# Performance work log

Hardware: AMD Instinct MI355X
Metric: run time of the kernel (lower is better)

## Reference

```python
import jax, jax.numpy as jnp
import numpy as np

N_NODES = 20000
N_EDGES = 160000
N_GRAPHS = 100
IN_CH = 64
EDGE_DIM = 8
NEG_SLOPE = 0.2


def _gatv2(x, edge_index, edge_attr, Wl, Wr, We, att, b, heads, ch, n_nodes):
    # GATv2Conv: e_ij = att . leaky_relu(Wl x_j + Wr x_i [+ We e_ij]), softmax over dst i,
    # out_i = sum_j alpha_ij * (Wl x_j), concat heads, + bias.
    src, dst = edge_index[0], edge_index[1]
    xl = (x @ Wl).reshape(-1, heads, ch)  # [N,H,C] source-side transform
    xr = (x @ Wr).reshape(-1, heads, ch)  # [N,H,C] target-side transform
    m = xl[src] + xr[dst]                 # [E,H,C]
    if edge_attr is not None:
        m = m + (edge_attr @ We).reshape(-1, heads, ch)
    m = jax.nn.leaky_relu(m, NEG_SLOPE)
    logit = jnp.einsum('ehc,hc->eh', m, att)                     # [E,H]
    mx = jax.ops.segment_max(logit, dst, num_segments=n_nodes)   # [N,H]
    ex = jnp.exp(logit - mx[dst])
    den = jax.ops.segment_sum(ex, dst, num_segments=n_nodes)     # [N,H]
    alpha = ex / (den[dst] + 1e-16)                              # [E,H]
    out = jax.ops.segment_sum(alpha[:, :, None] * xl[src], dst, num_segments=n_nodes)
    return out.reshape(-1, heads * ch) + b


def setup_inputs() -> dict:
    key = jax.random.key(0)
    ks = jax.random.split(key, 24)
    def rn(k, shape, fan_in):
        return jax.random.normal(k, shape, dtype=jnp.float32) / np.sqrt(fan_in)
    inp = {}
    inp['x'] = jax.random.normal(ks[0], (N_NODES, IN_CH), dtype=jnp.float32)
    inp['edge_attr'] = jax.random.uniform(ks[1], (N_EDGES, EDGE_DIM), dtype=jnp.float32)
    inp['Wl1'] = rn(ks[2], (IN_CH, 1024), IN_CH)
    inp['Wr1'] = rn(ks[3], (IN_CH, 1024), IN_CH)
    inp['We1'] = rn(ks[4], (EDGE_DIM, 1024), EDGE_DIM)
    inp['att1'] = rn(ks[5], (4, 256), 256)
    inp['b1'] = jnp.zeros((1024,), jnp.float32)
    inp['Wl2'] = rn(ks[6], (1024, 256), 1024)
    inp['Wr2'] = rn(ks[7], (1024, 256), 1024)
    inp['We2'] = rn(ks[8], (EDGE_DIM, 256), EDGE_DIM)
    inp['att2'] = rn(ks[9], (4, 64), 64)
    inp['b2'] = jnp.zeros((256,), jnp.float32)
    inp['Wlp'] = rn(ks[10], (256, 384), 256)
    inp['Wrp'] = rn(ks[11], (256, 384), 256)
    inp['attp'] = rn(ks[12], (6, 64), 64)
    inp['bp'] = jnp.zeros((384,), jnp.float32)
    inp['Wfc1'] = rn(ks[13], (384, 64), 384)
    inp['bfc1'] = jnp.zeros((64,), jnp.float32)
    inp['Wfc2'] = rn(ks[14], (64, 1), 64)
    inp['bfc2'] = jnp.zeros((1,), jnp.float32)
    inp['edge_index'] = jax.random.randint(ks[15], (2, N_EDGES), 0, N_NODES, dtype=jnp.int32)
    inp['edge_index_master'] = jax.random.randint(ks[16], (2, N_EDGES), 0, N_NODES, dtype=jnp.int32)
    inp['n_nodes'] = jnp.full((N_GRAPHS,), N_NODES // N_GRAPHS, dtype=jnp.int32)
    return inp


def reference(x, edge_attr, Wl1, Wr1, We1, att1, b1, Wl2, Wr2, We2, att2, b2,
              Wlp, Wrp, attp, bp, Wfc1, bfc1, Wfc2, bfc2,
              edge_index, edge_index_master, n_nodes):
    h = _gatv2(x, edge_index, edge_attr, Wl1, Wr1, We1, att1, b1, 4, 256, N_NODES)
    h = jax.nn.relu(h)
    h = _gatv2(h, edge_index, edge_attr, Wl2, Wr2, We2, att2, b2, 4, 64, N_NODES)
    h = jax.nn.relu(h)
    h = _gatv2(h, edge_index_master, None, Wlp, Wrp, None, attp, bp, 6, 64, N_NODES)
    last_idx = jnp.cumsum(n_nodes) - 1          # master node = last node of each graph
    master = h[last_idx]                        # [G,384] (dropout p=0 -> identity)
    z = jax.nn.relu(master @ Wfc1 + bfc1)
    return z @ Wfc2 + bfc2                      # [G,1]
```

## Files before the change

### kernel.cpp

```cpp
#include <hip/hip_runtime.h>
#include <hip/hip_bf16.h>

#define DIV_UP(a,b) (((a)+(b)-1)/(b))

typedef __attribute__((ext_vector_type(8))) short short8;
typedef __attribute__((ext_vector_type(4))) float floatx4;

static __device__ __forceinline__ unsigned short f2bf(float v) {
    unsigned u = __builtin_bit_cast(unsigned, v);
    u += 0x7fffu + ((u >> 16) & 1u);
    return (unsigned short)(u >> 16);
}
static __device__ __forceinline__ float bflo(unsigned v) {
    return __builtin_bit_cast(float, v << 16);
}
static __device__ __forceinline__ float bfhi(unsigned v) {
    return __builtin_bit_cast(float, v & 0xffff0000u);
}
static __device__ __forceinline__ float fexp2(float x) { return __builtin_amdgcn_exp2f(x); }
static __device__ __forceinline__ float f4get(const float4 v, int k) {
    return k == 0 ? v.x : k == 1 ? v.y : k == 2 ? v.z : v.w;
}

template <int CPL> struct RawT;
template <> struct RawT<8> { using T = uint4; };
template <> struct RawT<4> { using T = uint2; };
template <> struct RawT<2> { using T = unsigned; };

template <int CPL>
static __device__ __forceinline__ void unpackx(const typename RawT<CPL>::T& v, float* d) {
    if constexpr (CPL == 8) {
        d[0] = bflo(v.x); d[1] = bfhi(v.x);
        d[2] = bflo(v.y); d[3] = bfhi(v.y);
        d[4] = bflo(v.z); d[5] = bfhi(v.z);
        d[6] = bflo(v.w); d[7] = bfhi(v.w);
    } else if constexpr (CPL == 4) {
        d[0] = bflo(v.x); d[1] = bfhi(v.x);
        d[2] = bflo(v.y); d[3] = bfhi(v.y);
    } else {
        d[0] = bflo(v); d[1] = bfhi(v);
    }
}

template <int CPL>
static __device__ __forceinline__ void store_bf16v(unsigned short* p, const float* s) {
    unsigned short tmp[CPL];
#pragma unroll
    for (int c = 0; c < CPL; ++c) tmp[c] = f2bf(s[c]);
    if constexpr (CPL == 8) *(uint4*)p = *(uint4*)tmp;
    else if constexpr (CPL == 4) *(ushort4*)p = *(ushort4*)tmp;
    else if constexpr (CPL == 2) *(ushort2*)p = *(ushort2*)tmp;
    else p[0] = tmp[0];
}

template <int CTRL>
static __device__ __forceinline__ float dpp_mv(float x) {
    int r = __builtin_amdgcn_update_dpp(0, __builtin_bit_cast(int, x), CTRL, 0xF, 0xF, false);
    return __builtin_bit_cast(float, r);
}
template <int G>
static __device__ __forceinline__ float group_reduce(float x) {
    x += dpp_mv<0xB1>(x);
    x += dpp_mv<0x4E>(x);
    x += dpp_mv<0x124>(x);
    x += dpp_mv<0x128>(x);
    if constexpr (G >= 32) x += __shfl_xor(x, 16, 64);
    if constexpr (G >= 64) x += __shfl_xor(x, 32, 64);
    return x;
}

static __device__ __forceinline__ void tr_pair(const float* Wa, const float* Wb, int K, int Nn,
                                               unsigned short* Wt, int i) {
    int tot = K * Nn;
    const float* W = (i < tot) ? Wa : Wb;
    unsigned short* dst = Wt + ((i < tot) ? 0 : (size_t)Nn * K);
    int ii = (i < tot) ? i : i - tot;
    int k = ii % K, n = ii / K;
    dst[(size_t)n * K + k] = f2bf(W[(size_t)k * Nn + n]);
}

__global__ void prep_all(const float* __restrict__ x,
                         const float* __restrict__ Wl1, const float* __restrict__ Wr1,
                         const float* __restrict__ Wl2, const float* __restrict__ Wr2,
                         const float* __restrict__ Wlp, const float* __restrict__ Wrp,
                         unsigned short* __restrict__ xbf,
                         unsigned short* __restrict__ wt1, unsigned short* __restrict__ wt2,
                         unsigned short* __restrict__ wt3, int N) {
    const int S1 = 2 * 64 * 1024, S2 = 2 * 1024 * 256, S3 = 2 * 256 * 384;
    int id = blockIdx.x * blockDim.x + threadIdx.x;
    if (id < S1) tr_pair(Wl1, Wr1, 64, 1024, wt1, id);
    else if (id < S1 + S2) tr_pair(Wl2, Wr2, 1024, 256, wt2, id - S1);
    else if (id < S1 + S2 + S3) tr_pair(Wlp, Wrp, 256, 384, wt3, id - S1 - S2);
    else {
        int i = id - S1 - S2 - S3;
        if (i < N * 64) xbf[i] = f2bf(x[i]);
    }
}

#define GLOAD_LDS16(gp, lp) \
    __builtin_amdgcn_global_load_lds((const __attribute__((address_space(1))) void*)(gp), \
                                     (__attribute__((address_space(3))) void*)(lp), 16, 0, 0)

__global__ __launch_bounds__(256) void gemm_mfma(
    const unsigned short* __restrict__ A, const unsigned short* __restrict__ Bt,
    unsigned short* __restrict__ C, int M, int Ntot, int K) {
    __shared__ unsigned short As[128 * 32];
    __shared__ unsigned short Bs[128 * 32];
    const int tid = threadIdx.x;
    const int m0 = blockIdx.y * 128, n0 = blockIdx.x * 128;
    const int wave = tid >> 6, lane = tid & 63;
    const int wm = (wave >> 1) * 64, wn = (wave & 1) * 64;
    const int r15 = lane & 15, quad = lane >> 4;
    const int srow = lane >> 2, scol = (lane & 3) * 8;
    const int arow0 = m0 + 32 * wave + srow;
    const int brow0 = n0 + 32 * wave + srow;
    const unsigned short* ap0 = A + (size_t)arow0 * K + scol;
    const unsigned short* ap1 = ap0 + (size_t)16 * K;
    const unsigned short* bp0 = Bt + (size_t)brow0 * K + scol;
    const unsigned short* bp1 = bp0 + (size_t)16 * K;
    unsigned short* alds0 = As + (32 * wave) * 32;
    unsigned short* alds1 = alds0 + 16 * 32;
    unsigned short* blds0 = Bs + (32 * wave) * 32;
    unsigned short* blds1 = blds0 + 16 * 32;
    const bool av0 = arow0 < M, av1 = (arow0 + 16) < M;
    floatx4 acc[4][4];
#pragma unroll
    for (int i = 0; i < 4; ++i)
#pragma unroll
        for (int j = 0; j < 4; ++j) acc[i][j] = (floatx4)0.f;

    for (int k0 = 0; k0 < K; k0 += 32) {
        if (av0) GLOAD_LDS16(ap0, alds0);
        if (av1) GLOAD_LDS16(ap1, alds1);
        GLOAD_LDS16(bp0, blds0);
        GLOAD_LDS16(bp1, blds1);
        ap0 += 32; ap1 += 32; bp0 += 32; bp1 += 32;
        __syncthreads();
        short8 af[4], bfr[4];
#pragma unroll
        for (int i = 0; i < 4; ++i)
            af[i] = *(const short8*)(&As[(wm + i * 16 + r15) * 32 + quad * 8]);
#pragma unroll
        for (int j = 0; j < 4; ++j)
            bfr[j] = *(const short8*)(&Bs[(wn + j * 16 + r15) * 32 + quad * 8]);
#pragma unroll
        for (int i = 0; i < 4; ++i)
#pragma unroll
            for (int j = 0; j < 4; ++j)
                acc[i][j] = __builtin_amdgcn_mfma_f32_16x16x32_bf16(af[i], bfr[j], acc[i][j], 0, 0, 0);
        __syncthreads();
    }
#pragma unroll
    for (int i = 0; i < 4; ++i)
#pragma unroll
        for (int j = 0; j < 4; ++j)
#pragma unroll
            for (int r = 0; r < 4; ++r) {
                int m = m0 + wm + i * 16 + quad * 4 + r;
                int n = n0 + wn + j * 16 + r15;
                if (m < M) C[(size_t)m * Ntot + n] = f2bf(acc[i][j][r]);
            }
}

__global__ void count2_kernel(const int* __restrict__ dst0, const int* __restrict__ dst1,
                              int E, int N, int* __restrict__ cnt) {
    int e = blockIdx.x * blockDim.x + threadIdx.x;
    if (e < E) atomicAdd(&cnt[dst0[e]], 1);
    else if (e < 2 * E) atomicAdd(&cnt[N + dst1[e - E]], 1);
}

__global__ __launch_bounds__(1024) void scan_kernel(const int* __restrict__ cnt_all, int N,
                                                    int* __restrict__ off_all, int* __restrict__ cur_all) {
    const int* cnt = cnt_all + blockIdx.x * N;
    int* off = off_all + blockIdx.x * (N + 1);
    int* cur = cur_all + blockIdx.x * N;
    __shared__ int part[1024];
    int t = threadIdx.x;
    int per = (N + 1023) >> 10;
    int base = t * per;
    int s = 0;
    for (int i = 0; i < per; ++i) { int idx = base + i; if (idx < N) s += cnt[idx]; }
    part[t] = s;
    __syncthreads();
    for (int d2 = 1; d2 < 1024; d2 <<= 1) {
        int v = (t >= d2) ? part[t - d2] : 0;
        __syncthreads();
        part[t] += v;
        __syncthreads();
    }
    int pre = (t == 0) ? 0 : part[t - 1];
    for (int i = 0; i < per; ++i) {
        int idx = base + i;
        if (idx < N) { off[idx] = pre; cur[idx] = pre; pre += cnt[idx]; }
    }
    if (t == 1023) off[N] = part[1023];
}

__global__ void fill2_kernel(const int* __restrict__ src0, const int* __restrict__ dst0,
                             const int* __restrict__ src1, const int* __restrict__ dst1,
                             int E, int N, int* __restrict__ cur, int2* __restrict__ edges,
                             int* __restrict__ srcs) {
    int e = blockIdx.x * blockDim.x + threadIdx.x;
    if (e < E) {
        int p = atomicAdd(&cur[dst0[e]], 1);
        edges[p] = make_int2(src0[e], e);
        srcs[p] = src0[e];
    } else if (e < 2 * E) {
        int i = e - E;
        int p = atomicAdd(&cur[N + dst1[i]], 1);
        srcs[E + p] = src1[i];
    }
}

__global__ void ea_gather_kernel(const float* __restrict__ ea, const int2* __restrict__ edges,
                                 float* __restrict__ ead, int E) {
    int j = blockIdx.x * blockDim.x + threadIdx.x;
    if (j >= E) return;
    int ey = edges[j].y;
    const float4* s = (const float4*)(ea + (size_t)ey * 8);
    float4* o = (float4*)(ead + (size_t)j * 8);
    o[0] = s[0];
    o[1] = s[1];
}

template <int CPL, int NE>
struct EStage {
    int src[NE];
    typename RawT<CPL>::T xv[NE];
};

template <int D, int CPL, int NE>
static __device__ __forceinline__ void stage_x(
    const unsigned short* __restrict__ xlr, const int* __restrict__ srcs,
    int j, int c0, EStage<CPL, NE>& s) {
#pragma unroll
    for (int n = 0; n < NE; ++n) s.src[n] = srcs[j + n];
#pragma unroll
    for (int n = 0; n < NE; ++n)
        s.xv[n] = *(const typename RawT<CPL>::T*)(xlr + (size_t)s.src[n] * (2 * D) + c0);
}

template <int D, int CPL, int QP, int G, int NE>
static __device__ __forceinline__ void hase_compute(
    const EStage<CPL, NE>& s, const float* __restrict__ ead, int j,
    const float* wb, const float (&att_r)[CPL], const float (&xr_r)[CPL],
    float& m, float& l, float (&acc)[CPL]) {
    float4 evr[NE][2];
#pragma unroll
    for (int n = 0; n < NE; ++n) {
        const float4* q = (const float4*)(ead + (size_t)(j + n) * 8);
        evr[n][0] = q[0];
        evr[n][1] = q[1];
    }
    float z[NE][CPL];
#pragma unroll
    for (int n = 0; n < NE; ++n) {
        float xv[CPL];
        unpackx<CPL>(s.xv[n], xv);
#pragma unroll
        for (int c = 0; c < CPL; ++c) z[n][c] = xv[c] + xr_r[c];
    }
#pragma unroll
    for (int k = 0; k < 8; ++k) {
#pragma unroll
        for (int q = 0; q < CPL / 4; ++q) {
            float4 w4 = *(const float4*)(wb + k * D + q * QP);
#pragma unroll
            for (int n = 0; n < NE; ++n) {
                float ek = f4get(evr[n][k >> 2], k & 3);
                z[n][q * 4 + 0] = fmaf(ek, w4.x, z[n][q * 4 + 0]);
                z[n][q * 4 + 1] = fmaf(ek, w4.y, z[n][q * 4 + 1]);
                z[n][q * 4 + 2] = fmaf(ek, w4.z, z[n][q * 4 + 2]);
                z[n][q * 4 + 3] = fmaf(ek, w4.w, z[n][q * 4 + 3]);
            }
        }
    }
    float lg[NE];
#pragma unroll
    for (int n = 0; n < NE; ++n) {
        float t = 0.f;
#pragma unroll
        for (int c = 0; c < CPL; ++c) {
            float a = z[n][c] > 0.f ? z[n][c] : 0.2f * z[n][c];
            t = fmaf(att_r[c], a, t);
        }
        lg[n] = group_reduce<G>(t);
    }
    float mn = m;
#pragma unroll
    for (int n = 0; n < NE; ++n) mn = fmaxf(mn, lg[n]);
    float sc = fexp2(m - mn);
    float p[NE], ps = 0.f;
#pragma unroll
    for (int n = 0; n < NE; ++n) { p[n] = fexp2(lg[n] - mn); ps += p[n]; }
    m = mn;
    l = fmaf(l, sc, ps);
#pragma unroll
    for (int c = 0; c < CPL; ++c) acc[c] *= sc;
#pragma unroll
    for (int n = 0; n < NE; ++n) {
        float xv[CPL];
        unpackx<CPL>(s.xv[n], xv);
#pragma unroll
        for (int c = 0; c < CPL; ++c) acc[c] = fmaf(p[n], xv[c], acc[c]);
    }
}

template <int D, int C, int CB, int WPN, bool RELU>
__global__ __launch_bounds__(256) void attn_hase(
    const unsigned short* __restrict__ xlr, const float* __restrict__ ead,
    const float* __restrict__ We, const float* __restrict__ att,
    const int* __restrict__ srcs, const int* __restrict__ off,
    const float* __restrict__ bias, unsigned short* __restrict__ outp, int N) {
    constexpr int CPL = CB / 64;
    constexpr int HW = CB / C;
    constexpr int G = 64 / HW;
    constexpr int NPB = 4 / WPN;
    constexpr int QP = CB * 4 / CPL;
    __shared__ float wsh[8 * D];
    for (int f4 = threadIdx.x; f4 < 2 * D; f4 += 256) {
        int k = f4 / (D / 4);
        int c = (f4 - k * (D / 4)) * 4;
        int b = c / CB, cc = c - b * CB;
        int ln = cc / CPL, q = (cc % CPL) / 4;
        int dst = k * (D / 4) + (b * CB + q * QP + ln * 4) / 4;
        ((float4*)wsh)[dst] = ((const float4*)We)[f4];
    }
    __syncthreads();

    const int wid = threadIdx.x >> 6, lane = threadIdx.x & 63;
    const int wv = wid % WPN, wn = wid / WPN;
    const int c0 = wv * CB + lane * CPL;
    const float* wb = wsh + wv * CB + lane * 4;

    const float L2E = 1.4426950408889634f;
    float att_r[CPL];
#pragma unroll
    for (int c = 0; c < CPL; ++c) att_r[c] = att[c0 + c] * L2E;

    for (int node = blockIdx.x * NPB + wn; node < N; node += gridDim.x * NPB) {
        typename RawT<CPL>::T xrw =
            *(const typename RawT<CPL>::T*)(xlr + (size_t)node * (2 * D) + D + c0);
        float xr_r[CPL];
        unpackx<CPL>(xrw, xr_r);
        float m = -1e30f, l = 0.f, acc[CPL];
#pragma unroll
        for (int c = 0; c < CPL; ++c) acc[c] = 0.f;

        const int jb = __builtin_amdgcn_readfirstlane(off[node]);
        const int je = __builtin_amdgcn_readfirstlane(off[node + 1]);
        int j = jb;
        int g = (je - jb) >> 2;
        if (g > 0) {
            EStage<CPL, 4> A, B;
            stage_x<D, CPL, 4>(xlr, srcs, j, c0, A);
            while (g >= 2) {
                stage_x<D, CPL, 4>(xlr, srcs, j + 4, c0, B);
                hase_compute<D, CPL, QP, G, 4>(A, ead, j, wb, att_r, xr_r, m, l, acc);
                j += 4; --g;
                if (g >= 2) {
                    stage_x<D, CPL, 4>(xlr, srcs, j + 4, c0, A);
                    hase_compute<D, CPL, QP, G, 4>(B, ead, j, wb, att_r, xr_r, m, l, acc);
                    j += 4; --g;
                } else if (g == 1) {
                    hase_compute<D, CPL, QP, G, 4>(B, ead, j, wb, att_r, xr_r, m, l, acc);
                    j += 4; --g;
                }
            }
            if (g == 1) {
                hase_compute<D, CPL, QP, G, 4>(A, ead, j, wb, att_r, xr_r, m, l, acc);
                j += 4;
            }
        }
        for (; j < je; ++j) {
            EStage<CPL, 1> S;
            stage_x<D, CPL, 1>(xlr, srcs, j, c0, S);
            hase_compute<D, CPL, QP, G, 1>(S, ead, j, wb, att_r, xr_r, m, l, acc);
        }

        float inv = 1.f / (l + 1e-16f);
        float r[CPL];
#pragma unroll
        for (int c = 0; c < CPL; ++c) {
            r[c] = fmaf(acc[c], inv, bias[c0 + c]);
            if constexpr (RELU) r[c] = fmaxf(r[c], 0.f);
        }
        store_bf16v<CPL>(outp + (size_t)node * D + c0, r);
    }
}

template <int D, int CPL, int G, int NE>
static __device__ __forceinline__ void noe_compute(
    const EStage<CPL, NE>& s,
    const float (&att_r)[CPL], const float (&xr_r)[CPL],
    float& m, float& l, float (&acc)[CPL]) {
    float xv[NE][CPL], lg[NE];
#pragma unroll
    for (int n = 0; n < NE; ++n) unpackx<CPL>(s.xv[n], xv[n]);
#pragma unroll
    for (int n = 0; n < NE; ++n) {
        float t = 0.f;
#pragma unroll
        for (int c = 0; c < CPL; ++c) {
            float z = xv[n][c] + xr_r[c];
            z = z > 0.f ? z : 0.2f * z;
            t = fmaf(att_r[c], z, t);
        }
        lg[n] = group_reduce<G>(t);
    }
    float mn = m;
#pragma unroll
    for (int n = 0; n < NE; ++n) mn = fmaxf(mn, lg[n]);
    float sc = fexp2(m - mn);
    float p[NE], ps = 0.f;
#pragma unroll
    for (int n = 0; n < NE; ++n) { p[n] = fexp2(lg[n] - mn); ps += p[n]; }
    m = mn;
    l = fmaf(l, sc, ps);
#pragma unroll
    for (int c = 0; c < CPL; ++c) {
        float t = p[0] * xv[0][c];
#pragma unroll
        for (int n = 1; n < NE; ++n) t = fmaf(p[n], xv[n][c], t);
        acc[c] = fmaf(acc[c], sc, t);
    }
}

template <int D, int C, int CB, bool RELU>
static __device__ __forceinline__ void attn_wave3(
    const unsigned short* __restrict__ xlr, const float* __restrict__ att,
    const int* __restrict__ srcs, int jb, int je,
    const float* __restrict__ bias, float* __restrict__ outp,
    int node, int cb, int lane) {
    constexpr int CPL = CB / 64;
    constexpr int HW = CB / C;
    constexpr int G = 64 / HW;
    const int c0 = cb + lane * CPL;
    const float L2E = 1.4426950408889634f;

    typename RawT<CPL>::T xrw =
        *(const typename RawT<CPL>::T*)(xlr + (size_t)node * (2 * D) + D + c0);
    float xr_r[CPL], att_r[CPL];
    unpackx<CPL>(xrw, xr_r);
#pragma unroll
    for (int c = 0; c < CPL; ++c) att_r[c] = att[c0 + c] * L2E;

    float m = -1e30f, l = 0.f, acc[CPL];
#pragma unroll
    for (int c = 0; c < CPL; ++c) acc[c] = 0.f;

    int j = jb;
    int g = (je - jb) >> 2;
    if (g > 0) {
        EStage<CPL, 4> A, B;
        stage_x<D, CPL, 4>(xlr, srcs, j, c0, A);
        while (g >= 2) {
            stage_x<D, CPL, 4>(xlr, srcs, j + 4, c0, B);
            noe_compute<D, CPL, G, 4>(A, att_r, xr_r, m, l, acc);
            j += 4; --g;
            if (g >= 2) {
                stage_x<D, CPL, 4>(xlr, srcs, j + 4, c0, A);
                noe_compute<D, CPL, G, 4>(B, att_r, xr_r, m, l, acc);
                j += 4; --g;
            } else if (g == 1) {
                noe_compute<D, CPL, G, 4>(B, att_r, xr_r, m, l, acc);
                j += 4; --g;
            }
        }
        if (g == 1) {
            noe_compute<D, CPL, G, 4>(A, att_r, xr_r, m, l, acc);
            j += 4;
        }
    }
    for (; j < je; ++j) {
        EStage<CPL, 1> S;
        stage_x<D, CPL, 1>(xlr, srcs, j, c0, S);
        noe_compute<D, CPL, G, 1>(S, att_r, xr_r, m, l, acc);
    }

    float inv = 1.f / (l + 1e-16f);
    float* out = outp + (size_t)node * D + c0;
    float tmp[CPL];
#pragma unroll
    for (int c = 0; c < CPL; ++c) {
        float r = fmaf(acc[c], inv, bias[c0 + c]);
        if constexpr (RELU) r = fmaxf(r, 0.f);
        tmp[c] = r;
    }
    if constexpr (CPL == 4) *(float4*)out = *(float4*)tmp;
    else if constexpr (CPL == 2) *(float2*)out = *(float2*)tmp;
    else out[0] = tmp[0];
}

template <int D, int C, int CB0, int CB1, bool RELU>
__global__ __launch_bounds__(256) void attn_noe(
    const unsigned short* __restrict__ xlr, const float* __restrict__ att,
    const int* __restrict__ srcs, const int* __restrict__ off,
    const float* __restrict__ bias, float* __restrict__ outp, int N) {
    const int wid = threadIdx.x >> 6, lane = threadIdx.x & 63;
    const int gw = blockIdx.x * 4 + wid;
    const int node = gw >> 1, wv = gw & 1;
    if (node >= N) return;
    const int jb = __builtin_amdgcn_readfirstlane(off[node]);
    const int je = __builtin_amdgcn_readfirstlane(off[node + 1]);
    if (wv == 0)
        attn_wave3<D, C, CB0, RELU>(xlr, att, srcs, jb, je, bias, outp, node, 0, lane);
    else
        attn_wave3<D, C, CB1, RELU>(xlr, att, srcs, jb, je, bias, outp, node, CB0, lane);
}

__global__ void mlp_kernel(const float* __restrict__ h3, const int* __restrict__ nn,
                           const float* __restrict__ Wfc1, const float* __restrict__ bfc1,
                           const float* __restrict__ Wfc2, const float* __restrict__ bfc2,
                           float* __restrict__ out, int G) {
    int g = blockIdx.x, t = threadIdx.x;
    int s = 0;
    for (int k = 0; k <= g; ++k) s += nn[k];
    const float* row = h3 + (size_t)(s - 1) * 384;
    float z = bfc1[t];
    for (int k = 0; k < 384; ++k) z = fmaf(row[k], Wfc1[k * 64 + t], z);
    z = fmaxf(z, 0.f);
    float v = z * Wfc2[t];
#pragma unroll
    for (int o = 32; o; o >>= 1) v += __shfl_xor(v, o, 64);
    if (t == 0) out[g] = v + bfc2[0];
}

extern "C" void kernel_launch(void* const* d_in, const int* in_sizes, int n_in,
                              void* d_out, int out_size, void* d_ws, size_t ws_size,
                              hipStream_t stream) {
    const float* x    = (const float*)d_in[0];
    const float* ea   = (const float*)d_in[1];
    const float* Wl1  = (const float*)d_in[2];
    const float* Wr1  = (const float*)d_in[3];
    const float* We1  = (const float*)d_in[4];
    const float* att1 = (const float*)d_in[5];
    const float* b1   = (const float*)d_in[6];
    const float* Wl2  = (const float*)d_in[7];
    const float* Wr2  = (const float*)d_in[8];
    const float* We2  = (const float*)d_in[9];
    const float* att2 = (const float*)d_in[10];
    const float* b2   = (const float*)d_in[11];
    const float* Wlp  = (const float*)d_in[12];
    const float* Wrp  = (const float*)d_in[13];
    const float* attp = (const float*)d_in[14];
    const float* bp   = (const float*)d_in[15];
    const float* Wfc1 = (const float*)d_in[16];
    const float* bfc1 = (const float*)d_in[17];
    const float* Wfc2 = (const float*)d_in[18];
    const float* bfc2 = (const float*)d_in[19];
    const int* ei     = (const int*)d_in[20];
    const int* eim    = (const int*)d_in[21];
    const int* nn     = (const int*)d_in[22];

    const int N = in_sizes[0] / 64;
    const int E = in_sizes[20] / 2;
    const int G = in_sizes[22];
    const int* src1 = ei,  *dst1 = ei + E;
    const int* srcm = eim, *dstm = eim + E;

    char* w = (char*)d_ws;
    size_t o = 0;
    auto alloc = [&](size_t b) { size_t r = o; o += (b + 255) & ~(size_t)255; return r; };
    char* R1 = w + alloc((size_t)N * 2048 * 2);
    unsigned short* xlr1 = (unsigned short*)R1;
    unsigned short* xlr3 = (unsigned short*)R1;
    float* h3 = (float*)(R1 + (size_t)N * 768 * 2 + 256);
    unsigned short* h1   = (unsigned short*)(w + alloc((size_t)N * 1024 * 2));
    unsigned short* xlr2 = (unsigned short*)(w + alloc((size_t)N * 512 * 2));
    unsigned short* h2   = (unsigned short*)(w + alloc((size_t)N * 256 * 2));
    unsigned short* xbf  = (unsigned short*)(w + alloc((size_t)N * 64 * 2));
    unsigned short* wt1  = (unsigned short*)(w + alloc((size_t)2048 * 64 * 2));
    unsigned short* wt2  = (unsigned short*)(w + alloc((size_t)512 * 1024 * 2));
    unsigned short* wt3  = (unsigned short*)(w + alloc((size_t)768 * 256 * 2));
    int*  cnt   = (int*)(w + alloc((size_t)2 * N * 4));
    int*  off   = (int*)(w + alloc((size_t)2 * (N + 1) * 4));
    int*  cur   = (int*)(w + alloc((size_t)2 * N * 4));
    char* eReg  = w + alloc((size_t)2 * E * 8 + 4096);
    int2* edges = (int2*)eReg;
    int*  srcs  = (int*)(eReg + (size_t)E * 8);
    (void)ws_size; (void)n_in; (void)out_size;

    float* ead1 = (float*)xlr2;
    float* ead2 = (float*)h1;

    dim3 blk(256);

    {
        int tot = 2 * 64 * 1024 + 2 * 1024 * 256 + 2 * 256 * 384 + N * 64;
        prep_all<<<DIV_UP(tot, 256), blk, 0, stream>>>(x, Wl1, Wr1, Wl2, Wr2, Wlp, Wrp,
                                                       xbf, wt1, wt2, wt3, N);
    }

    hipMemsetAsync(cnt, 0, (size_t)2 * N * 4, stream);
    count2_kernel<<<DIV_UP(2 * E, 256), blk, 0, stream>>>(dst1, dstm, E, N, cnt);
    scan_kernel<<<2, 1024, 0, stream>>>(cnt, N, off, cur);
    fill2_kernel<<<DIV_UP(2 * E, 256), blk, 0, stream>>>(src1, dst1, srcm, dstm, E, N, cur,
                                                         edges, srcs);
    ea_gather_kernel<<<DIV_UP(E, 256), blk, 0, stream>>>(ea, edges, ead1, E);
    const int* off3 = off + (N + 1);
    const int* srcs3 = srcs + E;

    gemm_mfma<<<dim3(2048 / 128, DIV_UP(N, 128)), blk, 0, stream>>>(xbf, wt1, xlr1, N, 2048, 64);
    attn_hase<1024, 256, 512, 2, true><<<2560, blk, 0, stream>>>(
        xlr1, ead1, We1, att1, srcs, off, b1, h1, N);

    gemm_mfma<<<dim3(512 / 128, DIV_UP(N, 128)), blk, 0, stream>>>(h1, wt2, xlr2, N, 512, 1024);
    ea_gather_kernel<<<DIV_UP(E, 256), blk, 0, stream>>>(ea, edges, ead2, E);
    attn_hase<256, 64, 256, 1, true><<<1280, blk, 0, stream>>>(
        xlr2, ead2, We2, att2, srcs, off, b2, h2, N);

    gemm_mfma<<<dim3(768 / 128, DIV_UP(N, 128)), blk, 0, stream>>>(h2, wt3, xlr3, N, 768, 256);
    attn_noe<384, 64, 256, 128, false><<<DIV_UP(N, 2), blk, 0, stream>>>(
        xlr3, attp, srcs3, off3, bp, h3, N);

    mlp_kernel<<<G, 64, 0, stream>>>(h3, nn, Wfc1, bfc1, Wfc2, bfc2, (float*)d_out, G);
}
```

Baseline: 456.1 us.

## Use fp16 dot2 for edge-feature projection and drop software double-buffering

Edge attributes are packed to fp16 pairs in the gather kernel and the We weights are packed into fp16 pairs in shared memory. This lets the edge projection use v_dot2 instructions, halving both the FMA count and the edge-attribute bytes read. The explicit A/B staging pipeline in both attention kernels is replaced with simple 4-edge groups, and the rescale of the accumulator is fused with the weighted sum. This lowers register pressure and instruction count, at the cost of losing the manual gather prefetch and adding fp16 rounding of edge features and weights.

```diff
diff --git a/kernel.cpp b/kernel.cpp
--- a/kernel.cpp
+++ b/kernel.cpp
@@ -5,6 +5,7 @@
 
 typedef __attribute__((ext_vector_type(8))) short short8;
 typedef __attribute__((ext_vector_type(4))) float floatx4;
+typedef _Float16 half2t __attribute__((ext_vector_type(2)));
 
 static __device__ __forceinline__ unsigned short f2bf(float v) {
     unsigned u = __builtin_bit_cast(unsigned, v);
@@ -18,7 +19,16 @@
     return __builtin_bit_cast(float, v & 0xffff0000u);
 }
 static __device__ __forceinline__ float fexp2(float x) { return __builtin_amdgcn_exp2f(x); }
-static __device__ __forceinline__ float f4get(const float4 v, int k) {
+
+static __device__ __forceinline__ unsigned packh2(float lo, float hi) {
+    half2t h; h[0] = (_Float16)lo; h[1] = (_Float16)hi;
+    return __builtin_bit_cast(unsigned, h);
+}
+static __device__ __forceinline__ float fdot2(unsigned a, unsigned b, float c) {
+    return __builtin_amdgcn_fdot2(__builtin_bit_cast(half2t, a),
+                                  __builtin_bit_cast(half2t, b), c, false);
+}
+static __device__ __forceinline__ unsigned uget(const uint4 v, int k) {
     return k == 0 ? v.x : k == 1 ? v.y : k == 2 ? v.z : v.w;
 }
 
@@ -213,65 +223,53 @@
 }
 
 __global__ void ea_gather_kernel(const float* __restrict__ ea, const int2* __restrict__ edges,
-                                 float* __restrict__ ead, int E) {
+                                 uint4* __restrict__ ead, int E) {
     int j = blockIdx.x * blockDim.x + threadIdx.x;
     if (j >= E) return;
     int ey = edges[j].y;
     const float4* s = (const float4*)(ea + (size_t)ey * 8);
-    float4* o = (float4*)(ead + (size_t)j * 8);
-    o[0] = s[0];
-    o[1] = s[1];
-}
-
-template <int CPL, int NE>
-struct EStage {
+    float4 a = s[0], b = s[1];
+    uint4 o;
+    o.x = packh2(a.x, a.y);
+    o.y = packh2(a.z, a.w);
+    o.z = packh2(b.x, b.y);
+    o.w = packh2(b.z, b.w);
+    ead[j] = o;
+}
+
+template <int D, int CPL, int G, int NE>
+static __device__ __forceinline__ void hase_group(
+    const unsigned short* __restrict__ xlr, const uint4* __restrict__ ej,
+    const int* __restrict__ sj, const unsigned* wbu,
+    const float (&att_r)[CPL], const float (&xr_r)[CPL], int c0,
+    float& m, float& l, float (&acc)[CPL]) {
     int src[NE];
-    typename RawT<CPL>::T xv[NE];
-};
-
-template <int D, int CPL, int NE>
-static __device__ __forceinline__ void stage_x(
-    const unsigned short* __restrict__ xlr, const int* __restrict__ srcs,
-    int j, int c0, EStage<CPL, NE>& s) {
-#pragma unroll
-    for (int n = 0; n < NE; ++n) s.src[n] = srcs[j + n];
-#pragma unroll
-    for (int n = 0; n < NE; ++n)
-        s.xv[n] = *(const typename RawT<CPL>::T*)(xlr + (size_t)s.src[n] * (2 * D) + c0);
-}
-
-template <int D, int CPL, int QP, int G, int NE>
-static __device__ __forceinline__ void hase_compute(
-    const EStage<CPL, NE>& s, const float* __restrict__ ead, int j,
-    const float* wb, const float (&att_r)[CPL], const float (&xr_r)[CPL],
-    float& m, float& l, float (&acc)[CPL]) {
-    float4 evr[NE][2];
+#pragma unroll
+    for (int n = 0; n < NE; ++n) src[n] = sj[n];
+    uint4 ev[NE];
+#pragma unroll
+    for (int n = 0; n < NE; ++n) ev[n] = ej[n];
+    float xv[NE][CPL], z[NE][CPL];
 #pragma unroll
     for (int n = 0; n < NE; ++n) {
-        const float4* q = (const float4*)(ead + (size_t)(j + n) * 8);
-        evr[n][0] = q[0];
-        evr[n][1] = q[1];
-    }
-    float z[NE][CPL];
-#pragma unroll
-    for (int n = 0; n < NE; ++n) {
-        float xv[CPL];
-        unpackx<CPL>(s.xv[n], xv);
-#pragma unroll
-        for (int c = 0; c < CPL; ++c) z[n][c] = xv[c] + xr_r[c];
-    }
-#pragma unroll
-    for (int k = 0; k < 8; ++k) {
+        typename RawT<CPL>::T xw =
+            *(const typename RawT<CPL>::T*)(xlr + (size_t)src[n] * (2 * D) + c0);
+        unpackx<CPL>(xw, xv[n]);
+#pragma unroll
+        for (int c = 0; c < CPL; ++c) z[n][c] = xv[n][c] + xr_r[c];
+    }
+#pragma unroll
+    for (int kp = 0; kp < 4; ++kp) {
 #pragma unroll
         for (int q = 0; q < CPL / 4; ++q) {
-            float4 w4 = *(const float4*)(wb + k * D + q * QP);
+            uint4 w4 = *(const uint4*)(wbu + kp * D + q * 256);
 #pragma unroll
             for (int n = 0; n < NE; ++n) {
-                float ek = f4get(evr[n][k >> 2], k & 3);
-                z[n][q * 4 + 0] = fmaf(ek, w4.x, z[n][q * 4 + 0]);
-                z[n][q * 4 + 1] = fmaf(ek, w4.y, z[n][q * 4 + 1]);
-                z[n][q * 4 + 2] = fmaf(ek, w4.z, z[n][q * 4 + 2]);
-                z[n][q * 4 + 3] = fmaf(ek, w4.w, z[n][q * 4 + 3]);
+                unsigned ep = uget(ev[n], kp);
+                z[n][q * 4 + 0] = fdot2(ep, w4.x, z[n][q * 4 + 0]);
+                z[n][q * 4 + 1] = fdot2(ep, w4.y, z[n][q * 4 + 1]);
+                z[n][q * 4 + 2] = fdot2(ep, w4.z, z[n][q * 4 + 2]);
+                z[n][q * 4 + 3] = fdot2(ep, w4.w, z[n][q * 4 + 3]);
             }
         }
     }
@@ -296,19 +294,17 @@
     m = mn;
     l = fmaf(l, sc, ps);
 #pragma unroll
-    for (int c = 0; c < CPL; ++c) acc[c] *= sc;
-#pragma unroll
-    for (int n = 0; n < NE; ++n) {
-        float xv[CPL];
-        unpackx<CPL>(s.xv[n], xv);
-#pragma unroll
-        for (int c = 0; c < CPL; ++c) acc[c] = fmaf(p[n], xv[c], acc[c]);
+    for (int c = 0; c < CPL; ++c) {
+        float t = p[0] * xv[0][c];
+#pragma unroll
+        for (int n = 1; n < NE; ++n) t = fmaf(p[n], xv[n][c], t);
+        acc[c] = fmaf(acc[c], sc, t);
     }
 }
 
 template <int D, int C, int CB, int WPN, bool RELU>
 __global__ __launch_bounds__(256) void attn_hase(
-    const unsigned short* __restrict__ xlr, const float* __restrict__ ead,
+    const unsigned short* __restrict__ xlr, const uint4* __restrict__ ead4,
     const float* __restrict__ We, const float* __restrict__ att,
     const int* __restrict__ srcs, const int* __restrict__ off,
     const float* __restrict__ bias, unsigned short* __restrict__ outp, int N) {
@@ -316,22 +312,31 @@
     constexpr int HW = CB / C;
     constexpr int G = 64 / HW;
     constexpr int NPB = 4 / WPN;
-    constexpr int QP = CB * 4 / CPL;
-    __shared__ float wsh[8 * D];
-    for (int f4 = threadIdx.x; f4 < 2 * D; f4 += 256) {
-        int k = f4 / (D / 4);
-        int c = (f4 - k * (D / 4)) * 4;
-        int b = c / CB, cc = c - b * CB;
-        int ln = cc / CPL, q = (cc % CPL) / 4;
-        int dst = k * (D / 4) + (b * CB + q * QP + ln * 4) / 4;
-        ((float4*)wsh)[dst] = ((const float4*)We)[f4];
+    __shared__ unsigned wsh[4 * D];
+    for (int idx = threadIdx.x; idx < D; idx += 256) {
+        int kp = idx / (D / 4);
+        int t = idx - kp * (D / 4);
+        int pos = 4 * t;
+        int b = pos / CB;
+        int r = pos - b * CB;
+        int q = r >> 8;
+        int ln4 = r - (q << 8);
+        int cc = b * CB + (ln4 >> 2) * CPL + q * 4;
+        float4 w0 = *(const float4*)(We + (size_t)(2 * kp) * D + cc);
+        float4 w1 = *(const float4*)(We + (size_t)(2 * kp + 1) * D + cc);
+        uint4 o;
+        o.x = packh2(w0.x, w1.x);
+        o.y = packh2(w0.y, w1.y);
+        o.z = packh2(w0.z, w1.z);
+        o.w = packh2(w0.w, w1.w);
+        ((uint4*)wsh)[idx] = o;
     }
     __syncthreads();
 
     const int wid = threadIdx.x >> 6, lane = threadIdx.x & 63;
     const int wv = wid % WPN, wn = wid / WPN;
     const int c0 = wv * CB + lane * CPL;
-    const float* wb = wsh + wv * CB + lane * 4;
+    const unsigned* wbu = wsh + wv * CB + lane * 4;
 
     const float L2E = 1.4426950408889634f;
     float att_r[CPL];
@@ -350,33 +355,10 @@
         const int jb = __builtin_amdgcn_readfirstlane(off[node]);
         const int je = __builtin_amdgcn_readfirstlane(off[node + 1]);
         int j = jb;
-        int g = (je - jb) >> 2;
-        if (g > 0) {
-            EStage<CPL, 4> A, B;
-            stage_x<D, CPL, 4>(xlr, srcs, j, c0, A);
-            while (g >= 2) {
-                stage_x<D, CPL, 4>(xlr, srcs, j + 4, c0, B);
-                hase_compute<D, CPL, QP, G, 4>(A, ead, j, wb, att_r, xr_r, m, l, acc);
-                j += 4; --g;
-                if (g >= 2) {
-                    stage_x<D, CPL, 4>(xlr, srcs, j + 4, c0, A);
-                    hase_compute<D, CPL, QP, G, 4>(B, ead, j, wb, att_r, xr_r, m, l, acc);
-                    j += 4; --g;
-                } else if (g == 1) {
-                    hase_compute<D, CPL, QP, G, 4>(B, ead, j, wb, att_r, xr_r, m, l, acc);
-                    j += 4; --g;
-                }
-            }
-            if (g == 1) {
-                hase_compute<D, CPL, QP, G, 4>(A, ead, j, wb, att_r, xr_r, m, l, acc);
-                j += 4;
-            }
-        }
-        for (; j < je; ++j) {
-            EStage<CPL, 1> S;
-            stage_x<D, CPL, 1>(xlr, srcs, j, c0, S);
-            hase_compute<D, CPL, QP, G, 1>(S, ead, j, wb, att_r, xr_r, m, l, acc);
-        }
+        for (; j + 4 <= je; j += 4)
+            hase_group<D, CPL, G, 4>(xlr, ead4 + j, srcs + j, wbu, att_r, xr_r, c0, m, l, acc);
+        for (; j < je; ++j)
+            hase_group<D, CPL, G, 1>(xlr, ead4 + j, srcs + j, wbu, att_r, xr_r, c0, m, l, acc);
 
         float inv = 1.f / (l + 1e-16f);
         float r[CPL];
@@ -390,13 +372,20 @@
 }
 
 template <int D, int CPL, int G, int NE>
-static __device__ __forceinline__ void noe_compute(
-    const EStage<CPL, NE>& s,
-    const float (&att_r)[CPL], const float (&xr_r)[CPL],
+static __device__ __forceinline__ void noe_group(
+    const unsigned short* __restrict__ xlr, const int* __restrict__ sj,
+    const float (&att_r)[CPL], const float (&xr_r)[CPL], int c0,
     float& m, float& l, float (&acc)[CPL]) {
+    int src[NE];
+#pragma unroll
+    for (int n = 0; n < NE; ++n) src[n] = sj[n];
     float xv[NE][CPL], lg[NE];
 #pragma unroll
-    for (int n = 0; n < NE; ++n) unpackx<CPL>(s.xv[n], xv[n]);
+    for (int n = 0; n < NE; ++n) {
+        typename RawT<CPL>::T xw =
+            *(const typename RawT<CPL>::T*)(xlr + (size_t)src[n] * (2 * D) + c0);
+        unpackx<CPL>(xw, xv[n]);
+    }
 #pragma unroll
     for (int n = 0; n < NE; ++n) {
         float t = 0.f;
@@ -450,33 +439,10 @@
     for (int c = 0; c < CPL; ++c) acc[c] = 0.f;
 
     int j = jb;
-    int g = (je - jb) >> 2;
-    if (g > 0) {
-        EStage<CPL, 4> A, B;
-        stage_x<D, CPL, 4>(xlr, srcs, j, c0, A);
-        while (g >= 2) {
-            stage_x<D, CPL, 4>(xlr, srcs, j + 4, c0, B);
-            noe_compute<D, CPL, G, 4>(A, att_r, xr_r, m, l, acc);
-            j += 4; --g;
-            if (g >= 2) {
-                stage_x<D, CPL, 4>(xlr, srcs, j + 4, c0, A);
-                noe_compute<D, CPL, G, 4>(B, att_r, xr_r, m, l, acc);
-                j += 4; --g;
-            } else if (g == 1) {
-                noe_compute<D, CPL, G, 4>(B, att_r, xr_r, m, l, acc);
-                j += 4; --g;
-            }
-        }
-        if (g == 1) {
-            noe_compute<D, CPL, G, 4>(A, att_r, xr_r, m, l, acc);
-            j += 4;
-        }
-    }
-    for (; j < je; ++j) {
-        EStage<CPL, 1> S;
-        stage_x<D, CPL, 1>(xlr, srcs, j, c0, S);
-        noe_compute<D, CPL, G, 1>(S, att_r, xr_r, m, l, acc);
-    }
+    for (; j + 4 <= je; j += 4)
+        noe_group<D, CPL, G, 4>(xlr, srcs + j, att_r, xr_r, c0, m, l, acc);
+    for (; j < je; ++j)
+        noe_group<D, CPL, G, 1>(xlr, srcs + j, att_r, xr_r, c0, m, l, acc);
 
     float inv = 1.f / (l + 1e-16f);
     float* out = outp + (size_t)node * D + c0;
@@ -581,8 +547,8 @@
     int*  srcs  = (int*)(eReg + (size_t)E * 8);
     (void)ws_size; (void)n_in; (void)out_size;
 
-    float* ead1 = (float*)xlr2;
-    float* ead2 = (float*)h1;
+    uint4* ead1 = (uint4*)xlr2;
+    uint4* ead2 = (uint4*)h1;
 
     dim3 blk(256);
 
```

Measured after the change: 415.3 us. 8.9% less time.
